# Performance work log

Hardware: AMD Instinct MI355X
Metric: run time of the kernel (lower is better)

## Reference

```python
import jax, jax.numpy as jnp
import numpy as np

# AdaptiveLogSoftmaxWithLoss config (input_dim=2048, n_classes=50257, div_value=4.0)
CUTOFFS = [1000, 10000, 50257]  # torch appends n_classes
N_CLUSTERS = 2                   # len(CUTOFFS) - 1
HEAD_SIZE = CUTOFFS[0] + N_CLUSTERS  # 1002
D = 2048
HSZ = [D // 4, D // 16]          # tail hidden sizes: [512, 128]
N_TOK = 4096


def setup_inputs() -> dict:
    key = jax.random.key(0)
    ks = jax.random.split(key, 7)
    w = 0.02  # weight scale so logits stay O(1)
    x = jax.random.normal(ks[0], (N_TOK, D), dtype=jnp.float32)
    W_head = jax.random.normal(ks[1], (HEAD_SIZE, D), dtype=jnp.float32) * w
    W1_0 = jax.random.normal(ks[2], (HSZ[0], D), dtype=jnp.float32) * w
    W2_0 = jax.random.normal(ks[3], (CUTOFFS[1] - CUTOFFS[0], HSZ[0]), dtype=jnp.float32) * w  # [9000, 512]
    W1_1 = jax.random.normal(ks[4], (HSZ[1], D), dtype=jnp.float32) * w
    W2_1 = jax.random.normal(ks[5], (CUTOFFS[2] - CUTOFFS[1], HSZ[1]), dtype=jnp.float32) * w  # [40257, 128]
    target = jax.random.randint(ks[6], (N_TOK,), 0, CUTOFFS[2], dtype=jnp.int32)
    return {"x": x, "target": target, "W_head": W_head,
            "W1_0": W1_0, "W2_0": W2_0, "W1_1": W1_1, "W2_1": W2_1}


def reference(x, target, W_head, W1_0, W2_0, W1_1, W2_1):
    # head: [N, 1002] = [1000 frequent classes | 2 cluster logits]
    head = x @ W_head.T
    head_lsm = jax.nn.log_softmax(head, axis=-1)

    t = target
    # log-prob of target if it lies in the head (clip keeps gather in-range; masked later)
    head_lp = jnp.take_along_axis(head_lsm, jnp.clip(t, 0, CUTOFFS[0] - 1)[:, None], axis=1)[:, 0]

    def tail_target_lp(W1, W2, low, high, cluster_idx):
        # two-stage projection: [N,D] @ [D,h] @ [h,osz]
        logits = (x @ W1.T) @ W2.T                     # [N, high-low]
        lsm = jax.nn.log_softmax(logits, axis=-1)
        idx = jnp.clip(t - low, 0, high - low - 1)
        g = jnp.take_along_axis(lsm, idx[:, None], axis=1)[:, 0]
        # combine with head's cluster log-prob
        return head_lsm[:, CUTOFFS[0] + cluster_idx] + g

    lp0 = tail_target_lp(W1_0, W2_0, CUTOFFS[0], CUTOFFS[1], 0)
    lp1 = tail_target_lp(W1_1, W2_1, CUTOFFS[1], CUTOFFS[2], 1)

    out = jnp.where(t < CUTOFFS[0], head_lp, jnp.where(t < CUTOFFS[1], lp0, lp1))
    loss = -jnp.mean(out)
    return out, loss
```

## Files before the change

### kernel.cpp

```cpp
#include <hip/hip_runtime.h>
#include <hip/hip_bf16.h>
#include <math.h>

#define NTOK 4096
#define DIM 2048
#define NHEAD 1002
#define NCAT 1664
#define C0LO 1000
#define C0HI 10000
#define OSZ0 9000
#define OSZ1 40257
#define P0 9024
#define P1 40320
#define PAD0 24.0f
#define PAD1 63.0f
#define H0S 512
#define H1S 128
#define JS0 32
#define JS1 24
#define HEADBLKS 8
#define NT0 141
#define NT1 630
#define PROJB 416
#define CVTB 352

typedef __attribute__((ext_vector_type(4))) short short4v;
typedef __attribute__((ext_vector_type(8))) short short8v;
typedef __attribute__((ext_vector_type(4))) float f32x4;
typedef __hip_bfloat16 bf16;

#define GLOBAL_AS __attribute__((address_space(1)))
#define LDS_AS __attribute__((address_space(3)))

#define RAW_BAR() __builtin_amdgcn_s_barrier()
#define SCHED_FENCE() __builtin_amdgcn_sched_barrier(0)
#define WAIT_VM(N) asm volatile("s_waitcnt vmcnt(" #N ")" ::: "memory")
#define WAIT_LGKM0() asm volatile("s_waitcnt lgkmcnt(0)" ::: "memory")
#define PRIO(N) __builtin_amdgcn_s_setprio(N)

__device__ __forceinline__ int kperm(int c) {
  return (c & ~31) | (((c & 15) >> 2) << 3) | (((c >> 4) & 1) << 2) | (c & 3);
}

__device__ __forceinline__ void cvt8(const float* s1, const float* s2, bf16* dst) {
  union { short8v v; bf16 h[8]; } u;
  float4 a = *reinterpret_cast<const float4*>(s1);
  float4 b = *reinterpret_cast<const float4*>(s2);
  u.h[0] = __float2bfloat16(a.x); u.h[1] = __float2bfloat16(a.y);
  u.h[2] = __float2bfloat16(a.z); u.h[3] = __float2bfloat16(a.w);
  u.h[4] = __float2bfloat16(b.x); u.h[5] = __float2bfloat16(b.y);
  u.h[6] = __float2bfloat16(b.z); u.h[7] = __float2bfloat16(b.w);
  *reinterpret_cast<short8v*>(dst) = u.v;
}

__device__ __forceinline__ void zero8(bf16* dst) {
  union { short8v v; bf16 h[8]; } u;
#pragma unroll
  for (int e = 0; e < 8; ++e) u.h[e] = __float2bfloat16(0.f);
  *reinterpret_cast<short8v*>(dst) = u.v;
}

__global__ __launch_bounds__(256) void cvt_xw(
    const float* __restrict__ x, const float* __restrict__ W_head,
    const float* __restrict__ W1_0, const float* __restrict__ W1_1,
    bf16* __restrict__ xb, bf16* __restrict__ Wcat) {
  const long NX = (long)NTOK * DIM / 8;
  const long NC = (long)NCAT * DIM / 8;
  long gid = (long)blockIdx.x * 256 + threadIdx.x;
  if (gid < NX) {
    long rel = gid * 8;
    long c1 = (rel & ~31L) + ((rel >> 3) & 3) * 4;
    cvt8(x + c1, x + c1 + 16, xb + rel);
  } else if (gid < NX + NC) {
    long rel = (gid - NX) * 8;
    int row = (int)(rel >> 11);
    long c1 = (rel & ~31L) + ((rel >> 3) & 3) * 4;
    int col = (int)(c1 & 2047);
    const float* srow = nullptr;
    if (row < NHEAD) srow = W_head + (long)row * DIM;
    else if (row < 1024) srow = nullptr;
    else if (row < 1536) srow = W1_0 + (long)(row - 1024) * DIM;
    else srow = W1_1 + (long)(row - 1536) * DIM;
    if (srow) cvt8(srow + col, srow + col + 16, Wcat + rel);
    else      zero8(Wcat + rel);
  }
}

__device__ __forceinline__ void stage_tile(const bf16* __restrict__ g, int row0,
                                           int ld, int k0,
                                           char* lds, int wave, int lane) {
#pragma unroll
  for (int c = 0; c < 4; ++c) {
    int rbase = wave * 32 + c * 8;
    int row = rbase + (lane >> 3);
    int slot = (lane & 7) ^ (row & 7);
    const bf16* src = g + (size_t)(row0 + row) * ld + k0 + slot * 8;
    __builtin_amdgcn_global_load_lds((const GLOBAL_AS unsigned int*)src,
                                     (LDS_AS unsigned int*)(lds + rbase * 128),
                                     16, 0, 0);
  }
}

__device__ __forceinline__ void stage_tileB64(const bf16* __restrict__ g, int row0,
                                              int ld, int k0,
                                              char* lds, int wave, int lane) {
#pragma unroll
  for (int c = 0; c < 2; ++c) {
    int rbase = wave * 16 + c * 8;
    int row = rbase + (lane >> 3);
    int slot = (lane & 7) ^ (row & 7);
    const bf16* src = g + (size_t)(row0 + row) * ld + k0 + slot * 8;
    __builtin_amdgcn_global_load_lds((const GLOBAL_AS unsigned int*)src,
                                     (LDS_AS unsigned int*)(lds + rbase * 128),
                                     16, 0, 0);
  }
}

__device__ __forceinline__ void stage_tile256(const bf16* __restrict__ g, int row0,
                                              int ld, char* lds, int wave, int lane) {
#pragma unroll
  for (int c = 0; c < 8; ++c) {
    int rbase = wave * 32 + c * 4;
    int row = rbase + (lane >> 4);
    int slot = (lane & 15) ^ (row & 7);
    const bf16* src = g + (size_t)(row0 + row) * ld + slot * 8;
    __builtin_amdgcn_global_load_lds((const GLOBAL_AS unsigned int*)src,
                                     (LDS_AS unsigned int*)(lds + rbase * 256),
                                     16, 0, 0);
  }
}

__device__ __forceinline__ void stage_tile256_64(const bf16* __restrict__ g, int row0,
                                                 int ld, char* lds, int wave, int lane) {
#pragma unroll
  for (int c = 0; c < 4; ++c) {
    int rbase = wave * 16 + c * 4;
    int row = rbase + (lane >> 4);
    int slot = (lane & 15) ^ (row & 7);
    const bf16* src = g + (size_t)(row0 + row) * ld + slot * 8;
    __builtin_amdgcn_global_load_lds((const GLOBAL_AS unsigned int*)src,
                                     (LDS_AS unsigned int*)(lds + rbase * 256),
                                     16, 0, 0);
  }
}

__device__ __forceinline__ short8v read_frag(const char* lds, int row, int kk, int lane) {
  int slot = (kk * 4 + (lane >> 4)) ^ (row & 7);
  return *reinterpret_cast<const short8v*>(lds + row * 128 + slot * 16);
}
__device__ __forceinline__ short8v read_frag256(const char* lds, int row, int kk, int lane) {
  int slot = (kk * 4 + (lane >> 4)) ^ (row & 7);
  return *reinterpret_cast<const short8v*>(lds + row * 256 + slot * 16);
}

__device__ __forceinline__ void reduce_write_ps(float srun[4][4], float* reds,
                                                float* ps, int slice, int tok0,
                                                int lane, int wr, int wc) {
#pragma unroll
  for (int off = 1; off < 16; off <<= 1)
#pragma unroll
    for (int m = 0; m < 4; ++m)
#pragma unroll
      for (int r = 0; r < 4; ++r) srun[m][r] += __shfl_xor(srun[m][r], off);
  __syncthreads();
  if (wc == 0 && (lane & 15) == 0) {
#pragma unroll
    for (int m = 0; m < 4; ++m)
#pragma unroll
      for (int r = 0; r < 4; ++r)
        reds[wr * 64 + m * 16 + (lane >> 4) * 4 + r] = srun[m][r];
  }
  __syncthreads();
  if (wc == 1 && (lane & 15) == 0) {
#pragma unroll
    for (int m = 0; m < 4; ++m)
#pragma unroll
      for (int r = 0; r < 4; ++r) {
        int row = wr * 64 + m * 16 + (lane >> 4) * 4 + r;
        ps[(size_t)slice * NTOK + tok0 + row] = reds[row] + srun[m][r];
      }
  }
}

__global__ __launch_bounds__(256, 4) void tail0_lse(
    const bf16* __restrict__ Ab, const bf16* __restrict__ W2b,
    float* __restrict__ ps) {
  __shared__ __align__(16) char As[16384];
  __shared__ __align__(16) char Bs[8192];
  __shared__ float reds[128];
  int tid = threadIdx.x;
  int lane = tid & 63, wave = tid >> 6;
  int wr = wave >> 1, wc = wave & 1;
  int tok0 = blockIdx.x * 128;
  int ys = blockIdx.y;
  int t_lo = (NT0 * ys) / JS0, t_hi = (NT0 * (ys + 1)) / JS0;
  float srun[4][4] = {};
  for (int jt = t_lo; jt < t_hi; ++jt) {
    int j0 = jt * 64;
    f32x4 acc[4][2] = {};
    for (int k0 = 0; k0 < H0S; k0 += 64) {
      __syncthreads();
      stage_tile(Ab, tok0, H0S, k0, As, wave, lane);
      stage_tileB64(W2b, j0, H0S, k0, Bs, wave, lane);
      __syncthreads();
      PRIO(1);
#pragma unroll
      for (int kk = 0; kk < 2; ++kk) {
        short8v af[4], bfr[2];
#pragma unroll
        for (int m = 0; m < 4; ++m)
          af[m] = read_frag(As, wr * 64 + m * 16 + (lane & 15), kk, lane);
#pragma unroll
        for (int n = 0; n < 2; ++n)
          bfr[n] = read_frag(Bs, wc * 32 + n * 16 + (lane & 15), kk, lane);
#pragma unroll
        for (int m = 0; m < 4; ++m)
#pragma unroll
          for (int n = 0; n < 2; ++n)
            acc[m][n] = __builtin_amdgcn_mfma_f32_16x16x32_bf16(af[m], bfr[n], acc[m][n], 0, 0, 0);
      }
      PRIO(0);
    }
#pragma unroll
    for (int m = 0; m < 4; ++m)
#pragma unroll
      for (int n = 0; n < 2; ++n)
#pragma unroll
        for (int r = 0; r < 4; ++r) srun[m][r] += __expf(acc[m][n][r]);
  }
  reduce_write_ps(srun, reds, ps, ys, tok0, lane, wr, wc);
}

__device__ void tail1_body(const bf16* __restrict__ Ab, const bf16* __restrict__ W2b,
                           float* __restrict__ ps, char* lds) {
  char* buf0 = lds;
  char* buf1 = lds + 16384;
  float* reds = (float*)(lds + 32768);
  int tid = threadIdx.x;
  int lane = tid & 63, wave = tid >> 6;
  int wr = wave >> 1, wc = wave & 1;
  int tok0 = blockIdx.x * 128;
  int ys = blockIdx.y;
  int t_lo = (NT1 * ys) / JS1, t_hi = (NT1 * (ys + 1)) / JS1;
  int nt = t_hi - t_lo;

  stage_tile256(Ab, tok0, H1S, lds, wave, lane);
  WAIT_VM(0); SCHED_FENCE();
  RAW_BAR();
  short8v afr[4][4];
#pragma unroll
  for (int kk = 0; kk < 4; ++kk)
#pragma unroll
    for (int m = 0; m < 4; ++m)
      afr[kk][m] = read_frag256(lds, wr * 64 + m * 16 + (lane & 15), kk, lane);
  WAIT_LGKM0(); SCHED_FENCE();
  RAW_BAR();
  stage_tile256_64(W2b, t_lo * 64, H1S, buf0, wave, lane);
  if (nt > 1) stage_tile256_64(W2b, (t_lo + 1) * 64, H1S, buf1, wave, lane);

  float srun[4][4] = {};
  for (int i = 0; i < nt; ++i) {
    char* cur = (i & 1) ? buf1 : buf0;
    if (i + 1 < nt) { WAIT_VM(4); } else { WAIT_VM(0); }
    SCHED_FENCE();
    RAW_BAR();
    f32x4 acc[4][2] = {};
    PRIO(1);
#pragma unroll
    for (int kk = 0; kk < 4; ++kk) {
      short8v bfr[2];
#pragma unroll
      for (int n = 0; n < 2; ++n)
        bfr[n] = read_frag256(cur, wc * 32 + n * 16 + (lane & 15), kk, lane);
#pragma unroll
      for (int m = 0; m < 4; ++m)
#pragma unroll
        for (int n = 0; n < 2; ++n)
          acc[m][n] = __builtin_amdgcn_mfma_f32_16x16x32_bf16(afr[kk][m], bfr[n], acc[m][n], 0, 0, 0);
    }
    PRIO(0);
#pragma unroll
    for (int m = 0; m < 4; ++m)
#pragma unroll
      for (int n = 0; n < 2; ++n)
#pragma unroll
        for (int r = 0; r < 4; ++r) srun[m][r] += __expf(acc[m][n][r]);
    SCHED_FENCE();
    RAW_BAR();
    if (i + 2 < nt) stage_tile256_64(W2b, (t_lo + i + 2) * 64, H1S, cur, wave, lane);
  }
  reduce_write_ps(srun, reds, ps, ys, tok0, lane, wr, wc);
}

__global__ __launch_bounds__(256, 3) void tail1_lse(
    const bf16* __restrict__ Ab, const bf16* __restrict__ W2b,
    float* __restrict__ ps) {
  __shared__ __align__(16) char lds[33280];
  tail1_body(Ab, W2b, ps, lds);
}

__global__ __launch_bounds__(256, 3) void proj_plus(
    const bf16* __restrict__ A, const bf16* __restrict__ B,
    const float* __restrict__ W2_0, const float* __restrict__ W2_1,
    bf16* __restrict__ W20b, bf16* __restrict__ W21b,
    float* __restrict__ head, float* __restrict__ h0, bf16* __restrict__ h0b,
    float* __restrict__ h1, bf16* __restrict__ h1b, float* __restrict__ ps_head) {
  __shared__ __align__(16) char As[16384];
  __shared__ __align__(16) char Bs[16384];
  __shared__ float reds[128];
  if (blockIdx.x >= PROJB) {
    const long G20 = (long)P0 * H0S / 8;
    const long G21 = (long)P1 * H1S / 8;
    const long R20 = (long)OSZ0 * H0S / 8;
    const long R21 = (long)OSZ1 * H1S / 8;
    long idx = (long)(blockIdx.x - PROJB) * 256 + threadIdx.x;
    const long stride = (long)CVTB * 256;
    for (; idx < G20 + G21; idx += stride) {
      long rel; const float* srcb; bf16* dstb; bool real;
      if (idx < G20) { rel = idx * 8;          srcb = W2_0; dstb = W20b + rel; real = idx < R20; }
      else { long j = idx - G20; rel = j * 8;  srcb = W2_1; dstb = W21b + rel; real = j < R21; }
      if (real) {
        long c1 = (rel & ~31L) + ((rel >> 3) & 3) * 4;
        cvt8(srcb + c1, srcb + c1 + 16, dstb);
      } else {
        zero8(dstb);
      }
    }
    return;
  }
  int tid = threadIdx.x;
  int lane = tid & 63, wave = tid >> 6;
  int wr = wave >> 1, wc = wave & 1;
  int wgid = blockIdx.x;
  int cx = wgid & 7, w = wgid >> 3;
  int col_b = w >> 2;
  int row_b = cx * 4 + (w & 3);
  int row0 = row_b * 128, col0 = col_b * 128;
  f32x4 acc[4][4] = {};
  for (int k0 = 0; k0 < DIM; k0 += 64) {
    __syncthreads();
    stage_tile(A, row0, DIM, k0, As, wave, lane);
    stage_tile(B, col0, DIM, k0, Bs, wave, lane);
    __syncthreads();
#pragma unroll
    for (int kk = 0; kk < 2; ++kk) {
      short8v af[4], bfr[4];
#pragma unroll
      for (int m = 0; m < 4; ++m)
        af[m] = read_frag(As, wr * 64 + m * 16 + (lane & 15), kk, lane);
#pragma unroll
      for (int n = 0; n < 4; ++n)
        bfr[n] = read_frag(Bs, wc * 64 + n * 16 + (lane & 15), kk, lane);
#pragma unroll
      for (int m = 0; m < 4; ++m)
#pragma unroll
        for (int n = 0; n < 4; ++n)
          acc[m][n] = __builtin_amdgcn_mfma_f32_16x16x32_bf16(af[m], bfr[n], acc[m][n], 0, 0, 0);
    }
  }
  float srun[4][4] = {};
#pragma unroll
  for (int m = 0; m < 4; ++m) {
    int row = row0 + wr * 64 + m * 16 + (lane >> 4) * 4;
#pragma unroll
    for (int n = 0; n < 4; ++n) {
      int col = col0 + wc * 64 + n * 16 + (lane & 15);
#pragma unroll
      for (int r = 0; r < 4; ++r) {
        float v = acc[m][n][r];
        if (col < NHEAD) {
          head[(size_t)(row + r) * NHEAD + col] = v;
          srun[m][r] += __expf(v);
        } else if (col >= 1024 && col < 1536) {
          int c = col - 1024;
          h0[(size_t)(row + r) * H0S + c] = v;
          h0b[(size_t)(row + r) * H0S + kperm(c)] = __float2bfloat16(v);
        } else if (col >= 1536) {
          int c = col - 1536;
          h1[(size_t)(row + r) * H1S + c] = v;
          h1b[(size_t)(row + r) * H1S + kperm(c)] = __float2bfloat16(v);
        }
      }
    }
  }
  if (col_b < HEADBLKS) {
    reduce_write_ps(srun, reds, ps_head, col_b, row0, lane, wr, wc);
  }
}

__global__ __launch_bounds__(256) void finalize2(
    const int* __restrict__ target, const float* __restrict__ head,
    const float* __restrict__ ps_head,
    const float* __restrict__ h0, const float* __restrict__ h1,
    const float* __restrict__ W2_0, const float* __restrict__ W2_1,
    const float* __restrict__ ps0, const float* __restrict__ ps1,
    float* __restrict__ out) {
  int warp = threadIdx.x >> 6, lane = threadIdx.x & 63;
  int i = blockIdx.x * 4 + warp;
  if (i >= NTOK) return;
  int t = target[i];
  float sh = 0.f;
#pragma unroll
  for (int s = 0; s < HEADBLKS; ++s) sh += ps_head[(size_t)s * NTOK + i];
  float lse_head = logf(sh);
  float res;
  if (t < C0LO) {
    res = head[(size_t)i * NHEAD + t] - lse_head;
  } else {
    int c = (t < C0HI) ? 0 : 1;
    int H = c ? H1S : H0S;
    int low = c ? C0HI : C0LO;
    const float* hv = (c ? h1 : h0) + (size_t)i * H;
    const float* wv = (c ? W2_1 : W2_0) + (size_t)(t - low) * H;
    float p = 0.f;
    for (int k = lane * 4; k < H; k += 256) {
      float4 a = *reinterpret_cast<const float4*>(hv + k);
      float4 b = *reinterpret_cast<const float4*>(wv + k);
      p += a.x * b.x + a.y * b.y + a.z * b.z + a.w * b.w;
    }
#pragma unroll
    for (int off = 32; off > 0; off >>= 1) p += __shfl_xor(p, off);
    const float* ps = c ? ps1 : ps0;
    int js = c ? JS1 : JS0;
    float S = 0.f;
    for (int s = 0; s < js; ++s) S += ps[(size_t)s * NTOK + i];
    S -= c ? PAD1 : PAD0;
    float cl = head[(size_t)i * NHEAD + C0LO + c];
    res = (cl - lse_head) + (p - logf(S));
  }
  if (lane == 0) out[i] = res;
}

__global__ __launch_bounds__(256) void loss_kernel(float* __restrict__ out) {
  __shared__ float red[256];
  int tid = threadIdx.x;
  float s = 0.f;
  for (int j = tid; j < NTOK; j += 256) s += out[j];
  red[tid] = s; __syncthreads();
  for (int off = 128; off > 0; off >>= 1) {
    if (tid < off) red[tid] += red[tid + off];
    __syncthreads();
  }
  if (tid == 0) out[NTOK] = -red[0] / (float)NTOK;
}

extern "C" void kernel_launch(void* const* d_in, const int* in_sizes, int n_in,
                              void* d_out, int out_size, void* d_ws, size_t ws_size,
                              hipStream_t stream) {
  (void)in_sizes; (void)n_in; (void)out_size; (void)ws_size;
  const float* x = (const float*)d_in[0];
  const int* target = (const int*)d_in[1];
  const float* W_head = (const float*)d_in[2];
  const float* W1_0 = (const float*)d_in[3];
  const float* W2_0 = (const float*)d_in[4];
  const float* W1_1 = (const float*)d_in[5];
  const float* W2_1 = (const float*)d_in[6];
  float* out = (float*)d_out;

  char* w = (char*)d_ws;
  size_t off = 0;
  auto alloc = [&](size_t bytes) -> void* {
    void* p = w + off;
    off = (off + bytes + 255) & ~(size_t)255;
    return p;
  };
  bf16* xb   = (bf16*)alloc((size_t)NTOK * DIM * 2);
  bf16* Wcat = (bf16*)alloc((size_t)NCAT * DIM * 2);
  bf16* W20b = (bf16*)alloc((size_t)P0 * H0S * 2);
  bf16* W21b = (bf16*)alloc((size_t)P1 * H1S * 2);
  float* head = (float*)alloc((size_t)NTOK * NHEAD * 4);
  float* h0   = (float*)alloc((size_t)NTOK * H0S * 4);
  bf16*  h0b  = (bf16*)alloc((size_t)NTOK * H0S * 2);
  float* h1   = (float*)alloc((size_t)NTOK * H1S * 4);
  bf16*  h1b  = (bf16*)alloc((size_t)NTOK * H1S * 2);
  float* ps_head = (float*)alloc((size_t)HEADBLKS * NTOK * 4);
  float* ps0 = (float*)alloc((size_t)JS0 * NTOK * 4);
  float* ps1 = (float*)alloc((size_t)JS1 * NTOK * 4);

  dim3 blk(256);
  const long NXW = (long)NTOK * DIM / 8 + (long)NCAT * DIM / 8;
  cvt_xw<<<dim3((unsigned)((NXW + 255) / 256)), blk, 0, stream>>>(
      x, W_head, W1_0, W1_1, xb, Wcat);

  proj_plus<<<dim3(PROJB + CVTB), blk, 0, stream>>>(
      xb, Wcat, W2_0, W2_1, W20b, W21b, head, h0, h0b, h1, h1b, ps_head);

  tail0_lse<<<dim3(NTOK / 128, JS0), blk, 0, stream>>>(h0b, W20b, ps0);
  tail1_lse<<<dim3(NTOK / 128, JS1), blk, 0, stream>>>(h1b, W21b, ps1);

  finalize2<<<dim3(NTOK / 4), blk, 0, stream>>>(target, head, ps_head, h0, h1,
                                                W2_0, W2_1, ps0, ps1, out);
  loss_kernel<<<1, blk, 0, stream>>>(out);
}
```

Before: 168.4 us.

## Merge tail LSE kernels into one launch and store head/hidden only in bf16

The two tail log-sum-exp kernels become one launch that dispatches on block index, so both tails share the GPU and one launch is saved. The projection epilogue stops writing fp32 copies of the head logits and the hidden activations, writing only bf16 (head padded to stride 1008). Finalize reads the bf16 copies and undoes the k-permutation when pairing with the fp32 W2 rows. This cuts global write traffic, at the cost of bf16 precision in the target logit and dot product, and of a fused kernel running at the larger LDS footprint.

```diff
diff --git a/kernel.cpp b/kernel.cpp
--- a/kernel.cpp
+++ b/kernel.cpp
@@ -5,6 +5,7 @@
 #define NTOK 4096
 #define DIM 2048
 #define NHEAD 1002
+#define HB_STRIDE 1008
 #define NCAT 1664
 #define C0LO 1000
 #define C0HI 10000
@@ -18,6 +19,7 @@
 #define H1S 128
 #define JS0 32
 #define JS1 24
+#define NB0 1024
 #define HEADBLKS 8
 #define NT0 141
 #define NT1 630
@@ -182,17 +184,16 @@
   }
 }
 
-__global__ __launch_bounds__(256, 4) void tail0_lse(
-    const bf16* __restrict__ Ab, const bf16* __restrict__ W2b,
-    float* __restrict__ ps) {
-  __shared__ __align__(16) char As[16384];
-  __shared__ __align__(16) char Bs[8192];
-  __shared__ float reds[128];
+__device__ void tail0_body(const bf16* __restrict__ Ab, const bf16* __restrict__ W2b,
+                           float* __restrict__ ps, int bid, char* lds) {
+  char* As = lds;
+  char* Bs = lds + 16384;
+  float* reds = (float*)(lds + 24576);
   int tid = threadIdx.x;
   int lane = tid & 63, wave = tid >> 6;
   int wr = wave >> 1, wc = wave & 1;
-  int tok0 = blockIdx.x * 128;
-  int ys = blockIdx.y;
+  int tok0 = (bid & 31) * 128;
+  int ys = bid >> 5;
   int t_lo = (NT0 * ys) / JS0, t_hi = (NT0 * (ys + 1)) / JS0;
   float srun[4][4] = {};
   for (int jt = t_lo; jt < t_hi; ++jt) {
@@ -232,15 +233,15 @@
 }
 
 __device__ void tail1_body(const bf16* __restrict__ Ab, const bf16* __restrict__ W2b,
-                           float* __restrict__ ps, char* lds) {
+                           float* __restrict__ ps, int bid, char* lds) {
   char* buf0 = lds;
   char* buf1 = lds + 16384;
   float* reds = (float*)(lds + 32768);
   int tid = threadIdx.x;
   int lane = tid & 63, wave = tid >> 6;
   int wr = wave >> 1, wc = wave & 1;
-  int tok0 = blockIdx.x * 128;
-  int ys = blockIdx.y;
+  int tok0 = (bid & 31) * 128;
+  int ys = bid >> 5;
   int t_lo = (NT1 * ys) / JS1, t_hi = (NT1 * (ys + 1)) / JS1;
   int nt = t_hi - t_lo;
 
@@ -292,19 +293,22 @@
   reduce_write_ps(srun, reds, ps, ys, tok0, lane, wr, wc);
 }
 
-__global__ __launch_bounds__(256, 3) void tail1_lse(
-    const bf16* __restrict__ Ab, const bf16* __restrict__ W2b,
-    float* __restrict__ ps) {
+__global__ __launch_bounds__(256, 4) void tails_fused(
+    const bf16* __restrict__ h0b, const bf16* __restrict__ W20b,
+    const bf16* __restrict__ h1b, const bf16* __restrict__ W21b,
+    float* __restrict__ ps0, float* __restrict__ ps1) {
   __shared__ __align__(16) char lds[33280];
-  tail1_body(Ab, W2b, ps, lds);
+  int bid = blockIdx.x;
+  if (bid < NB0) tail0_body(h0b, W20b, ps0, bid, lds);
+  else           tail1_body(h1b, W21b, ps1, bid - NB0, lds);
 }
 
 __global__ __launch_bounds__(256, 3) void proj_plus(
     const bf16* __restrict__ A, const bf16* __restrict__ B,
     const float* __restrict__ W2_0, const float* __restrict__ W2_1,
     bf16* __restrict__ W20b, bf16* __restrict__ W21b,
-    float* __restrict__ head, float* __restrict__ h0, bf16* __restrict__ h0b,
-    float* __restrict__ h1, bf16* __restrict__ h1b, float* __restrict__ ps_head) {
+    bf16* __restrict__ head_b, bf16* __restrict__ h0b, bf16* __restrict__ h1b,
+    float* __restrict__ ps_head) {
   __shared__ __align__(16) char As[16384];
   __shared__ __align__(16) char Bs[16384];
   __shared__ float reds[128];
@@ -369,16 +373,12 @@
       for (int r = 0; r < 4; ++r) {
         float v = acc[m][n][r];
         if (col < NHEAD) {
-          head[(size_t)(row + r) * NHEAD + col] = v;
+          head_b[(size_t)(row + r) * HB_STRIDE + col] = __float2bfloat16(v);
           srun[m][r] += __expf(v);
         } else if (col >= 1024 && col < 1536) {
-          int c = col - 1024;
-          h0[(size_t)(row + r) * H0S + c] = v;
-          h0b[(size_t)(row + r) * H0S + kperm(c)] = __float2bfloat16(v);
+          h0b[(size_t)(row + r) * H0S + kperm(col - 1024)] = __float2bfloat16(v);
         } else if (col >= 1536) {
-          int c = col - 1536;
-          h1[(size_t)(row + r) * H1S + c] = v;
-          h1b[(size_t)(row + r) * H1S + kperm(c)] = __float2bfloat16(v);
+          h1b[(size_t)(row + r) * H1S + kperm(col - 1536)] = __float2bfloat16(v);
         }
       }
     }
@@ -389,9 +389,9 @@
 }
 
 __global__ __launch_bounds__(256) void finalize2(
-    const int* __restrict__ target, const float* __restrict__ head,
+    const int* __restrict__ target, const bf16* __restrict__ head_b,
     const float* __restrict__ ps_head,
-    const float* __restrict__ h0, const float* __restrict__ h1,
+    const bf16* __restrict__ h0b, const bf16* __restrict__ h1b,
     const float* __restrict__ W2_0, const float* __restrict__ W2_1,
     const float* __restrict__ ps0, const float* __restrict__ ps1,
     float* __restrict__ out) {
@@ -405,18 +405,28 @@
   float lse_head = logf(sh);
   float res;
   if (t < C0LO) {
-    res = head[(size_t)i * NHEAD + t] - lse_head;
+    res = __bfloat162float(head_b[(size_t)i * HB_STRIDE + t]) - lse_head;
   } else {
     int c = (t < C0HI) ? 0 : 1;
     int H = c ? H1S : H0S;
     int low = c ? C0HI : C0LO;
-    const float* hv = (c ? h1 : h0) + (size_t)i * H;
+    const bf16* hv = (c ? h1b : h0b) + (size_t)i * H;
     const float* wv = (c ? W2_1 : W2_0) + (size_t)(t - low) * H;
     float p = 0.f;
     for (int k = lane * 4; k < H; k += 256) {
-      float4 a = *reinterpret_cast<const float4*>(hv + k);
-      float4 b = *reinterpret_cast<const float4*>(wv + k);
-      p += a.x * b.x + a.y * b.y + a.z * b.z + a.w * b.w;
+      int j = (k >> 2) & 7;
+      int chunk = k & ~31;
+      int wk = chunk + ((j & 1) << 4) + ((j >> 1) << 2);
+      ushort4 hraw = *reinterpret_cast<const ushort4*>(
+          reinterpret_cast<const unsigned short*>(hv) + k);
+      float4 b = *reinterpret_cast<const float4*>(wv + wk);
+      union { unsigned int u; float f; } cv;
+      float hx, hy, hz, hw;
+      cv.u = (unsigned int)hraw.x << 16; hx = cv.f;
+      cv.u = (unsigned int)hraw.y << 16; hy = cv.f;
+      cv.u = (unsigned int)hraw.z << 16; hz = cv.f;
+      cv.u = (unsigned int)hraw.w << 16; hw = cv.f;
+      p += hx * b.x + hy * b.y + hz * b.z + hw * b.w;
     }
 #pragma unroll
     for (int off = 32; off > 0; off >>= 1) p += __shfl_xor(p, off);
@@ -425,7 +435,7 @@
     float S = 0.f;
     for (int s = 0; s < js; ++s) S += ps[(size_t)s * NTOK + i];
     S -= c ? PAD1 : PAD0;
-    float cl = head[(size_t)i * NHEAD + C0LO + c];
+    float cl = __bfloat162float(head_b[(size_t)i * HB_STRIDE + C0LO + c]);
     res = (cl - lse_head) + (p - logf(S));
   }
   if (lane == 0) out[i] = res;
@@ -464,15 +474,13 @@
     off = (off + bytes + 255) & ~(size_t)255;
     return p;
   };
-  bf16* xb   = (bf16*)alloc((size_t)NTOK * DIM * 2);
-  bf16* Wcat = (bf16*)alloc((size_t)NCAT * DIM * 2);
-  bf16* W20b = (bf16*)alloc((size_t)P0 * H0S * 2);
-  bf16* W21b = (bf16*)alloc((size_t)P1 * H1S * 2);
-  float* head = (float*)alloc((size_t)NTOK * NHEAD * 4);
-  float* h0   = (float*)alloc((size_t)NTOK * H0S * 4);
-  bf16*  h0b  = (bf16*)alloc((size_t)NTOK * H0S * 2);
-  float* h1   = (float*)alloc((size_t)NTOK * H1S * 4);
-  bf16*  h1b  = (bf16*)alloc((size_t)NTOK * H1S * 2);
+  bf16* xb     = (bf16*)alloc((size_t)NTOK * DIM * 2);
+  bf16* Wcat   = (bf16*)alloc((size_t)NCAT * DIM * 2);
+  bf16* W20b   = (bf16*)alloc((size_t)P0 * H0S * 2);
+  bf16* W21b   = (bf16*)alloc((size_t)P1 * H1S * 2);
+  bf16* head_b = (bf16*)alloc((size_t)NTOK * HB_STRIDE * 2);
+  bf16* h0b    = (bf16*)alloc((size_t)NTOK * H0S * 2);
+  bf16* h1b    = (bf16*)alloc((size_t)NTOK * H1S * 2);
   float* ps_head = (float*)alloc((size_t)HEADBLKS * NTOK * 4);
   float* ps0 = (float*)alloc((size_t)JS0 * NTOK * 4);
   float* ps1 = (float*)alloc((size_t)JS1 * NTOK * 4);
@@ -483,12 +491,13 @@
       x, W_head, W1_0, W1_1, xb, Wcat);
 
   proj_plus<<<dim3(PROJB + CVTB), blk, 0, stream>>>(
-      xb, Wcat, W2_0, W2_1, W20b, W21b, head, h0, h0b, h1, h1b, ps_head);
-
-  tail0_lse<<<dim3(NTOK / 128, JS0), blk, 0, stream>>>(h0b, W20b, ps0);
-  tail1_lse<<<dim3(NTOK / 128, JS1), blk, 0, stream>>>(h1b, W21b, ps1);
-
-  finalize2<<<dim3(NTOK / 4), blk, 0, stream>>>(target, head, ps_head, h0, h1,
-                                                W2_0, W2_1, ps0, ps1, out);
+      xb, Wcat, W2_0, W2_1, W20b, W21b, head_b, h0b, h1b, ps_head);
+
+  tails_fused<<<dim3(NB0 + 32 * JS1), blk, 0, stream>>>(
+      h0b, W20b, h1b, W21b, ps0, ps1);
+
+  finalize2<<<dim3(NTOK / 4), blk, 0, stream>>>(target, head_b, ps_head,
+                                                h0b, h1b, W2_0, W2_1,
+                                                ps0, ps1, out);
   loss_kernel<<<1, blk, 0, stream>>>(out);
 }
```

Result: slower. 221.3 us (+31.4%).
